# Optimization experiments

Hardware: AMD Instinct MI355X
Metric: run time of the kernel (lower is better)

## Reference

```python
import jax, jax.numpy as jnp
import numpy as np

NQ = 4
NL = 3
# Z-expectation sign table: state axis order = wire order, reshape(-1) => wire 0 is MSB
_bits = (np.arange(2 ** NQ)[:, None] >> np.arange(NQ - 1, -1, -1)) & 1
Z_SIGNS = jnp.asarray((1 - 2 * _bits).astype(np.float32))  # (16, 4)
_CNOT = jnp.asarray(np.array([[1, 0, 0, 0], [0, 1, 0, 0], [0, 0, 0, 1], [0, 0, 1, 0]],
                             dtype=np.complex64).reshape(2, 2, 2, 2))


def _rx(t):
    c = jnp.cos(t / 2).astype(jnp.complex64)
    s = (-1j) * jnp.sin(t / 2).astype(jnp.complex64)
    return jnp.stack([jnp.stack([c, s]), jnp.stack([s, c])])


def _rot(phi, theta, omega):
    # PennyLane Rot = RZ(omega) @ RY(theta) @ RZ(phi)
    ez = jnp.exp(-0.5j * phi.astype(jnp.complex64))
    zero = jnp.zeros_like(ez)
    rz1 = jnp.stack([jnp.stack([ez, zero]), jnp.stack([zero, jnp.conj(ez)])])
    c = jnp.cos(theta / 2).astype(jnp.complex64)
    s = jnp.sin(theta / 2).astype(jnp.complex64)
    ry = jnp.stack([jnp.stack([c, -s]), jnp.stack([s, c])])
    eo = jnp.exp(-0.5j * omega.astype(jnp.complex64))
    rz2 = jnp.stack([jnp.stack([eo, zero]), jnp.stack([zero, jnp.conj(eo)])])
    return rz2 @ ry @ rz1


def _apply1(state, U, wire):
    state = jnp.tensordot(U, state, axes=[[1], [wire]])
    return jnp.moveaxis(state, 0, wire)


def _apply_cnot(state, c, t):
    state = jnp.tensordot(_CNOT, state, axes=[[2, 3], [c, t]])
    return jnp.moveaxis(state, [0, 1], [c, t])


def _circuit(x4, qw):
    state = jnp.zeros((2,) * NQ, jnp.complex64).at[(0,) * NQ].set(1.0)
    for i in range(NQ):
        state = _apply1(state, _rx(x4[i]), i)
    for layer in range(NL):
        for q in range(NQ):
            state = _apply1(state, _rot(qw[layer, q, 0], qw[layer, q, 1], qw[layer, q, 2]), q)
        for q in range(NQ - 1):
            state = _apply_cnot(state, q, q + 1)
    probs = jnp.abs(state.reshape(-1)) ** 2  # (16,)
    return probs @ Z_SIGNS  # (NQ,) PauliZ expectations


def setup_inputs() -> dict:
    key = jax.random.key(0)
    ks = jax.random.split(key, 16)
    D, H1, H2, L = 2048, 128, 64, 32
    B = 16384
    s = 0.02
    return {
        "x": jax.random.normal(ks[0], (B, D), jnp.float32),
        "enc_w0": jax.random.normal(ks[1], (D, H1), jnp.float32) * s,
        "enc_b0": jnp.zeros((H1,), jnp.float32),
        "enc_w1": jax.random.normal(ks[2], (H1, H2), jnp.float32) * s,
        "enc_b1": jnp.zeros((H2,), jnp.float32),
        "enc_w2": jax.random.normal(ks[3], (H2, L), jnp.float32) * s,
        "enc_b2": jnp.zeros((L,), jnp.float32),
        "qw": jax.random.normal(ks[4], (NL, NQ, 3), jnp.float32),
        "dec_w0": jax.random.normal(ks[5], (NQ, H2), jnp.float32) * s,
        "dec_b0": jnp.zeros((H2,), jnp.float32),
        "dec_w1": jax.random.normal(ks[6], (H2, H1), jnp.float32) * s,
        "dec_b1": jnp.zeros((H1,), jnp.float32),
        "dec_w2": jax.random.normal(ks[7], (H1, D), jnp.float32) * s,
        "dec_b2": jnp.zeros((D,), jnp.float32),
    }


def reference(x, enc_w0, enc_b0, enc_w1, enc_b1, enc_w2, enc_b2, qw,
              dec_w0, dec_b0, dec_w1, dec_b1, dec_w2, dec_b2):
    # Encoder (eval mode: dropout is identity)
    h = jax.nn.relu(x @ enc_w0 + enc_b0)
    h = jax.nn.relu(h @ enc_w1 + enc_b1)
    latent = h @ enc_w2 + enc_b2  # (B, 32)
    # Quantum refinement: circuit only reads latent[:, :NQ]
    refined = jax.vmap(lambda xi: _circuit(xi, qw))(latent[:, :NQ]).astype(jnp.float32)  # (B, 4)
    # Decoder
    h = jax.nn.relu(refined @ dec_w0 + dec_b0)
    h = jax.nn.relu(h @ dec_w1 + dec_b1)
    return h @ dec_w2 + dec_b2
```

## Files before the change

### kernel.cpp

```cpp
#include <hip/hip_runtime.h>
#include <hip/hip_bf16.h>

typedef __attribute__((ext_vector_type(8))) short short8;
typedef __attribute__((ext_vector_type(4))) float f32x4;

#define DEVI __device__ __forceinline__

DEVI unsigned short f2bf(float f) {
    union { float f; unsigned u; } v; v.f = f;
    unsigned r = v.u + 0x7FFFu + ((v.u >> 16) & 1u);
    return (unsigned short)(r >> 16);
}

DEVI unsigned cvtpk_bf16(float lo, float hi) {
    float2 t; t.x = lo; t.y = hi;
    __hip_bfloat162 h = __float22bfloat162_rn(t);
    union { __hip_bfloat162 h; unsigned u; } c; c.h = h;
    return c.u;
}

DEVI void gload_lds16(const void* g, void* l) {
    __builtin_amdgcn_global_load_lds(
        (const __attribute__((address_space(1))) unsigned int*)(unsigned long long)g,
        (__attribute__((address_space(3))) unsigned int*)(unsigned int)(unsigned long long)l,
        16, 0, 0);
}

DEVI void run_circuit(const float lat[4], const float* __restrict__ qw, float out4[4])
{
    float cw[4], sw[4];
#pragma unroll
    for (int w = 0; w < 4; ++w) sincosf(0.5f * lat[w], &sw[w], &cw[w]);

    float sr[16], si[16];
#pragma unroll
    for (int s = 0; s < 16; ++s) {
        float mag = 1.f; int p = 0;
#pragma unroll
        for (int w = 0; w < 4; ++w) {
            int b = (s >> (3 - w)) & 1;
            mag *= b ? sw[w] : cw[w];
            p += b;
        }
        p &= 3;
        sr[s] = (p == 0) ? mag : ((p == 2) ? -mag : 0.f);
        si[s] = (p == 1) ? -mag : ((p == 3) ? mag : 0.f);
    }

#pragma unroll
    for (int L = 0; L < 3; ++L) {
#pragma unroll
        for (int q = 0; q < 4; ++q) {
            const float* gq = qw + (L * 4 + q) * 3;
            float phi = gq[0], th = gq[1], om = gq[2];
            float ct, st;
            sincosf(0.5f * th, &st, &ct);
            float ap = 0.5f * (phi + om), am = 0.5f * (phi - om);
            float cap, sap, cam, sam;
            sincosf(ap, &sap, &cap);
            sincosf(am, &sam, &cam);
            float u00r =  ct * cap, u00i = -ct * sap;
            float u01r = -st * cam, u01i = -st * sam;
            float u10r =  st * cam, u10i = -st * sam;
            float u11r =  ct * cap, u11i =  ct * sap;
            int bm = 8 >> q;
#pragma unroll
            for (int i = 0; i < 16; ++i) {
                if (i & bm) continue;
                int j = i | bm;
                float ar = sr[i], ai = si[i], br = sr[j], bi = si[j];
                sr[i] = u00r*ar - u00i*ai + u01r*br - u01i*bi;
                si[i] = u00r*ai + u00i*ar + u01r*bi + u01i*br;
                sr[j] = u10r*ar - u10i*ai + u11r*br - u11i*bi;
                si[j] = u10r*ai + u10i*ar + u11r*bi + u11i*br;
            }
        }
#pragma unroll
        for (int q = 0; q < 3; ++q) {
            int cm = 8 >> q, tm = 8 >> (q + 1);
#pragma unroll
            for (int i = 0; i < 16; ++i) {
                if ((i & cm) && !(i & tm)) {
                    int j = i | tm;
                    float tr = sr[i]; sr[i] = sr[j]; sr[j] = tr;
                    float ti = si[i]; si[i] = si[j]; si[j] = ti;
                }
            }
        }
    }
#pragma unroll
    for (int q = 0; q < 4; ++q) {
        int bm = 8 >> q;
        float e = 0.f;
#pragma unroll
        for (int i = 0; i < 16; ++i) {
            float p = sr[i]*sr[i] + si[i]*si[i];
            e += (i & bm) ? -p : p;
        }
        out4[q] = e;
    }
}

__global__ void prep_kernel(const float* __restrict__ ew0, const float* __restrict__ ew1,
                            const float* __restrict__ dw1, const float* __restrict__ dw2,
                            unsigned short* __restrict__ wsb)
{
    int i = blockIdx.x * 256 + threadIdx.x;
    if (i < 262144) {
        int n = i >> 11, k = i & 2047;
        wsb[i] = f2bf(ew0[k * 128 + n]);
    } else if (i < 270336) {
        int t = i - 262144; int n = t >> 7, k = t & 127;
        wsb[i] = f2bf(ew1[k * 64 + n]);
    } else if (i < 278528) {
        int t = i - 270336; int n = t >> 6, k = t & 63;
        wsb[i] = f2bf(dw1[k * 128 + n]);
    } else if (i < 540672) {
        int t = i - 278528; int n = t >> 7, k = t & 127;
        wsb[i] = f2bf(dw2[k * 2048 + n]);
    }
}

__launch_bounds__(256, 2)
__global__ void enc_a_kernel(const float* __restrict__ x,
                             const unsigned short* __restrict__ w0T,
                             const float* __restrict__ b0g,
                             unsigned short* __restrict__ h1)
{
    __shared__ __align__(16) char smem[49152];

    const int tid = threadIdx.x;
    const int lane = tid & 63;
    const int wv = tid >> 6;
    const int wm = wv >> 1, wn = wv & 1;
    const int l16 = lane & 15, lq = lane >> 4;
    const int m0 = blockIdx.x * 32;

    const int rA0 = wv * 8 + (lane >> 4);
    const int rA1 = wv * 8 + 4 + (lane >> 4);
    const int slA0 = (lane & 15) ^ ((rA0 & 7) << 1);
    const int slA1 = (lane & 15) ^ ((rA1 & 7) << 1);
    const char* sA0 = (const char*)(x + (long)(m0 + rA0) * 2048 + slA0 * 4);
    const char* sA1 = (const char*)(x + (long)(m0 + rA1) * 2048 + slA1 * 4);
    const int rB0 = wv * 32 +  0 + (lane >> 3);
    const int rB1 = wv * 32 +  8 + (lane >> 3);
    const int rB2 = wv * 32 + 16 + (lane >> 3);
    const int rB3 = wv * 32 + 24 + (lane >> 3);
    const char* sB0 = (const char*)(w0T + rB0 * 2048 + ((lane & 7) ^ (rB0 & 7)) * 8);
    const char* sB1 = (const char*)(w0T + rB1 * 2048 + ((lane & 7) ^ (rB1 & 7)) * 8);
    const char* sB2 = (const char*)(w0T + rB2 * 2048 + ((lane & 7) ^ (rB2 & 7)) * 8);
    const char* sB3 = (const char*)(w0T + rB3 * 2048 + ((lane & 7) ^ (rB3 & 7)) * 8);
    const int aoff0 = wv * 2048;
    const int aoff1 = wv * 2048 + 1024;
    const int boff0 = wv * 4096;
    const int boff1 = wv * 4096 + 1024;
    const int boff2 = wv * 4096 + 2048;
    const int boff3 = wv * 4096 + 3072;

    auto issue = [&](int cur) {
        char* Ab = smem + (cur ? 8192 : 0);
        char* Bb = smem + (cur ? 32768 : 16384);
        gload_lds16(sA0, Ab + aoff0); sA0 += 256;
        gload_lds16(sA1, Ab + aoff1); sA1 += 256;
        gload_lds16(sB0, Bb + boff0); sB0 += 128;
        gload_lds16(sB1, Bb + boff1); sB1 += 128;
        gload_lds16(sB2, Bb + boff2); sB2 += 128;
        gload_lds16(sB3, Bb + boff3); sB3 += 128;
    };

    f32x4 acc[4];
#pragma unroll
    for (int b = 0; b < 4; ++b) acc[b] = (f32x4)(0.f);

    const int arow = wm * 16 + l16;
    const unsigned aswz = (unsigned)((arow & 7) << 1);

    issue(0);
    __syncthreads();

    for (int t = 0; t < 32; ++t) {
        if (t < 31) issue((t + 1) & 1);
        const char* Ab = smem + ((t & 1) ? 8192 : 0);
        const char* Bb = smem + ((t & 1) ? 32768 : 16384);
#pragma unroll
        for (int kk = 0; kk < 2; ++kk) {
            const int c = kk * 8 + lq * 2;
            const char* ap = Ab + arow * 256 + (((unsigned)c ^ aswz) << 4);
            float4 f0 = *(const float4*)ap;
            float4 f1 = *(const float4*)(ap + 16);
            union { unsigned u[4]; short8 s; } pk;
            pk.u[0] = cvtpk_bf16(f0.x, f0.y);
            pk.u[1] = cvtpk_bf16(f0.z, f0.w);
            pk.u[2] = cvtpk_bf16(f1.x, f1.y);
            pk.u[3] = cvtpk_bf16(f1.z, f1.w);
            short8 aF = pk.s;
#pragma unroll
            for (int fn = 0; fn < 4; ++fn) {
                int n = wn * 64 + fn * 16 + l16;
                short8 bF = *(const short8*)(Bb + n * 128 + (((kk * 4 + lq) ^ (n & 7)) << 4));
                acc[fn] = __builtin_amdgcn_mfma_f32_16x16x32_bf16(aF, bF, acc[fn], 0, 0, 0);
            }
        }
        __syncthreads();
    }

    float b0v[4];
#pragma unroll
    for (int fn = 0; fn < 4; ++fn) b0v[fn] = b0g[wn * 64 + fn * 16 + l16];
#pragma unroll
    for (int fn = 0; fn < 4; ++fn)
#pragma unroll
        for (int r = 0; r < 4; ++r) {
            int row = m0 + wm * 16 + lq * 4 + r;
            int col = wn * 64 + fn * 16 + l16;
            h1[row * 128 + col] = f2bf(fmaxf(acc[fn][r] + b0v[fn], 0.f));
        }
}

__launch_bounds__(256, 2)
__global__ void enc_b_kernel(const unsigned short* __restrict__ h1,
                             const unsigned short* __restrict__ w1eT,
                             const float* __restrict__ b1e,
                             const float* __restrict__ w2e,
                             const float* __restrict__ b2e,
                             const float* __restrict__ qw,
                             const float* __restrict__ w0d,
                             const float* __restrict__ b0d,
                             const unsigned short* __restrict__ w1dT,
                             const float* __restrict__ b1d,
                             unsigned short* __restrict__ g)
{
    __shared__ __align__(16) char smem[76288];
    char* const HA   = smem;
    char* const W1E  = smem + 16384;
    char* const W1D  = smem + 32768;
    float* const H2  = (float*)(smem + 49152);
    char* const HD   = smem + 65792;
    float* const W2C = (float*)(smem + 73984);
    float* const W0D = (float*)(smem + 75008);
    float* const B0D = (float*)(smem + 76032);

    const int tid = threadIdx.x;
    const int lane = tid & 63;
    const int wv = tid >> 6;
    const int wm = wv >> 1, wn = wv & 1;
    const int l16 = lane & 15, lq = lane >> 4;
    const int m0 = blockIdx.x * 64;

    {
        const int r16 = wv * 16 + (lane >> 4);
        const int s16 = lane & 15;
        const int r8  = wv * 32 + (lane >> 3);
        const int s8  = lane & 7;
#pragma unroll
        for (int i = 0; i < 4; ++i) {
            int row = r16 + i * 4;
            gload_lds16(h1 + (m0 + row) * 128 + ((s16 ^ (row & 7)) * 8),
                        HA + wv * 4096 + i * 1024);
        }
#pragma unroll
        for (int i = 0; i < 4; ++i) {
            int row = r16 + i * 4;
            gload_lds16(w1eT + row * 128 + ((s16 ^ (row & 7)) * 8),
                        W1E + wv * 4096 + i * 1024);
        }
#pragma unroll
        for (int i = 0; i < 4; ++i) {
            int row = r8 + i * 8;
            gload_lds16(w1dT + row * 64 + ((s8 ^ (row & 7)) * 8),
                        W1D + wv * 4096 + i * 1024);
        }
    }
    W2C[tid] = w2e[(tid >> 2) * 32 + (tid & 3)];
    W0D[tid] = w0d[tid];
    if (tid < 64) B0D[tid] = b0d[tid];
    __syncthreads();

    f32x4 acc2[2][2];
#pragma unroll
    for (int a = 0; a < 2; ++a)
#pragma unroll
        for (int b = 0; b < 2; ++b) acc2[a][b] = (f32x4)(0.f);
#pragma unroll
    for (int kk = 0; kk < 4; ++kk) {
        short8 aF[2], bF[2];
#pragma unroll
        for (int fm = 0; fm < 2; ++fm) {
            int row = wm * 32 + fm * 16 + l16;
            aF[fm] = *(const short8*)(HA + row * 256 + (((kk * 4 + lq) ^ (row & 7)) << 4));
        }
#pragma unroll
        for (int fn = 0; fn < 2; ++fn) {
            int n = wn * 32 + fn * 16 + l16;
            bF[fn] = *(const short8*)(W1E + n * 256 + (((kk * 4 + lq) ^ (n & 7)) << 4));
        }
#pragma unroll
        for (int fm = 0; fm < 2; ++fm)
#pragma unroll
            for (int fn = 0; fn < 2; ++fn)
                acc2[fm][fn] = __builtin_amdgcn_mfma_f32_16x16x32_bf16(aF[fm], bF[fn], acc2[fm][fn], 0, 0, 0);
    }
    {
        float b1v[2];
#pragma unroll
        for (int fn = 0; fn < 2; ++fn) b1v[fn] = b1e[wn * 32 + fn * 16 + l16];
#pragma unroll
        for (int fm = 0; fm < 2; ++fm)
#pragma unroll
            for (int fn = 0; fn < 2; ++fn)
#pragma unroll
                for (int r = 0; r < 4; ++r) {
                    int row = wm * 32 + fm * 16 + lq * 4 + r;
                    int col = wn * 32 + fn * 16 + l16;
                    H2[row * 65 + col] = fmaxf(acc2[fm][fn][r] + b1v[fn], 0.f);
                }
    }
    __syncthreads();

    if (tid < 64) {
        float lat[4];
#pragma unroll
        for (int j = 0; j < 4; ++j) lat[j] = b2e[j];
        const float* h2row = H2 + tid * 65;
#pragma unroll 8
        for (int k = 0; k < 64; ++k) {
            float hv = h2row[k];
#pragma unroll
            for (int j = 0; j < 4; ++j) lat[j] = fmaf(hv, W2C[k * 4 + j], lat[j]);
        }
        float o4[4];
        run_circuit(lat, qw, o4);
#pragma unroll
        for (int s = 0; s < 8; ++s) {
            uint4 pk;
            unsigned tmp[4];
#pragma unroll
            for (int p = 0; p < 4; ++p) {
                int c0 = s * 8 + p * 2;
                float v0 = fmaxf(o4[0]*W0D[c0]     + o4[1]*W0D[64+c0]   + o4[2]*W0D[128+c0]   + o4[3]*W0D[192+c0]   + B0D[c0],   0.f);
                float v1 = fmaxf(o4[0]*W0D[c0+1]   + o4[1]*W0D[64+c0+1] + o4[2]*W0D[128+c0+1] + o4[3]*W0D[192+c0+1] + B0D[c0+1], 0.f);
                tmp[p] = (unsigned)f2bf(v0) | ((unsigned)f2bf(v1) << 16);
            }
            pk.x = tmp[0]; pk.y = tmp[1]; pk.z = tmp[2]; pk.w = tmp[3];
            *(uint4*)(HD + tid * 128 + ((s ^ (tid & 7)) << 4)) = pk;
        }
    }
    __syncthreads();

    f32x4 accg[2][4];
#pragma unroll
    for (int a = 0; a < 2; ++a)
#pragma unroll
        for (int b = 0; b < 4; ++b) accg[a][b] = (f32x4)(0.f);
#pragma unroll
    for (int kk = 0; kk < 2; ++kk) {
        short8 aF[2], bF[4];
#pragma unroll
        for (int fm = 0; fm < 2; ++fm) {
            int row = wm * 32 + fm * 16 + l16;
            aF[fm] = *(const short8*)(HD + row * 128 + (((kk * 4 + lq) ^ (row & 7)) << 4));
        }
#pragma unroll
        for (int fn = 0; fn < 4; ++fn) {
            int n = wn * 64 + fn * 16 + l16;
            bF[fn] = *(const short8*)(W1D + n * 128 + (((kk * 4 + lq) ^ (n & 7)) << 4));
        }
#pragma unroll
        for (int fm = 0; fm < 2; ++fm)
#pragma unroll
            for (int fn = 0; fn < 4; ++fn)
                accg[fm][fn] = __builtin_amdgcn_mfma_f32_16x16x32_bf16(aF[fm], bF[fn], accg[fm][fn], 0, 0, 0);
    }
    {
        float b1v[4];
#pragma unroll
        for (int fn = 0; fn < 4; ++fn) b1v[fn] = b1d[wn * 64 + fn * 16 + l16];
#pragma unroll
        for (int fm = 0; fm < 2; ++fm)
#pragma unroll
            for (int fn = 0; fn < 4; ++fn)
#pragma unroll
                for (int r = 0; r < 4; ++r) {
                    int row = wm * 32 + fm * 16 + lq * 4 + r;
                    int col = wn * 64 + fn * 16 + l16;
                    g[(m0 + row) * 128 + col] = f2bf(fmaxf(accg[fm][fn][r] + b1v[fn], 0.f));
                }
    }
}

__launch_bounds__(256, 2)
__global__ void dec_b_kernel(const unsigned short* __restrict__ g,
                             const unsigned short* __restrict__ w2T,
                             const float* __restrict__ b2g,
                             float* __restrict__ out)
{
    __shared__ __align__(16) char smem[49152];
    char* const GA = smem;
    char* const WB = smem + 16384;

    const int tid = threadIdx.x;
    const int lane = tid & 63;
    const int wv = tid >> 6;
    const int wm = wv >> 1, wn = wv & 1;
    const int l16 = lane & 15, lq = lane >> 4;
    const int bid = blockIdx.x;
    const int n0 = (bid & 15) * 128;
    const int m0 = (bid >> 4) * 64;

    {
        const int rl = (lane >> 4);
        const int s16 = lane & 15;
#pragma unroll
        for (int i = 0; i < 4; ++i) {
            int row = wv * 16 + i * 4 + rl;
            gload_lds16(g + (m0 + row) * 128 + ((s16 ^ (row & 7)) * 8),
                        GA + wv * 4096 + i * 1024);
        }
#pragma unroll
        for (int i = 0; i < 8; ++i) {
            int row = wv * 32 + i * 4 + rl;
            gload_lds16(w2T + (n0 + row) * 128 + ((s16 ^ (row & 7)) * 8),
                        WB + wv * 8192 + i * 1024);
        }
    }
    __syncthreads();

    f32x4 a3[2][4];
#pragma unroll
    for (int a = 0; a < 2; ++a)
#pragma unroll
        for (int b = 0; b < 4; ++b) a3[a][b] = (f32x4)(0.f);
#pragma unroll
    for (int kk = 0; kk < 4; ++kk) {
        short8 aF[2], bF[4];
#pragma unroll
        for (int fm = 0; fm < 2; ++fm) {
            int row = wm * 32 + fm * 16 + l16;
            aF[fm] = *(const short8*)(GA + row * 256 + (((kk * 4 + lq) ^ (row & 7)) << 4));
        }
#pragma unroll
        for (int fn = 0; fn < 4; ++fn) {
            int n = wn * 64 + fn * 16 + l16;
            bF[fn] = *(const short8*)(WB + n * 256 + (((kk * 4 + lq) ^ (n & 7)) << 4));
        }
#pragma unroll
        for (int fm = 0; fm < 2; ++fm)
#pragma unroll
            for (int fn = 0; fn < 4; ++fn)
                a3[fm][fn] = __builtin_amdgcn_mfma_f32_16x16x32_bf16(aF[fm], bF[fn], a3[fm][fn], 0, 0, 0);
    }
    float b2v[4];
#pragma unroll
    for (int fn = 0; fn < 4; ++fn) b2v[fn] = b2g[n0 + wn * 64 + fn * 16 + l16];
#pragma unroll
    for (int fm = 0; fm < 2; ++fm)
#pragma unroll
        for (int fn = 0; fn < 4; ++fn)
#pragma unroll
            for (int r = 0; r < 4; ++r) {
                int row = m0 + wm * 32 + fm * 16 + lq * 4 + r;
                int col = n0 + wn * 64 + fn * 16 + l16;
                out[(long)row * 2048 + col] = a3[fm][fn][r] + b2v[fn];
            }
}

__launch_bounds__(256, 1)
__global__ void enc_kernel(const float* __restrict__ x,
                           const unsigned short* __restrict__ w0T,
                           const unsigned short* __restrict__ w1T,
                           const float* __restrict__ b0g,
                           const float* __restrict__ b1g,
                           const float* __restrict__ w2g,
                           const float* __restrict__ b2g,
                           const float* __restrict__ qw,
                           float* __restrict__ refined)
{
    __shared__ __align__(16) char smem[50432];
    char* const Abuf0 = smem;
    char* const Abuf1 = smem + 8192;
    char* const Bbuf0 = smem + 16384;
    char* const Bbuf1 = smem + 32768;
    char* const H1 = smem;
    char* const W1 = smem + 16384;
    float* const H2 = (float*)(smem + 32768);
    float* const W2C = (float*)(smem + 49408);

    const int tid = threadIdx.x;
    const int lane = tid & 63;
    const int wv = tid >> 6;
    const int wm = wv >> 1, wn = wv & 1;
    const int l16 = lane & 15, lq = lane >> 4;
    const int m0 = blockIdx.x * 64;

    const int ar = tid >> 4;
    const int ac4 = tid & 15;
    const int bn = tid >> 3;
    const int bs = tid & 7;

    const float* xg = x + m0 * 2048;
    W2C[tid] = w2g[(tid >> 2) * 32 + (tid & 3)];

    f32x4 acc[2][4];
#pragma unroll
    for (int a = 0; a < 2; ++a)
#pragma unroll
        for (int b = 0; b < 4; ++b) acc[a][b] = (f32x4)(0.f);

    float4 aL[4];
    uint4 bL[4];

    auto issue_loads = [&](int k0) {
#pragma unroll
        for (int j = 0; j < 4; ++j)
            aL[j] = *(const float4*)(xg + (ar + 16 * j) * 2048 + k0 + ac4 * 4);
#pragma unroll
        for (int j = 0; j < 4; ++j)
            bL[j] = *(const uint4*)(w0T + (bn + 32 * j) * 2048 + k0 + bs * 8);
    };
    auto write_lds = [&](int buf) {
        char* A = buf ? Abuf1 : Abuf0;
        char* B = buf ? Bbuf1 : Bbuf0;
#pragma unroll
        for (int j = 0; j < 4; ++j) {
            int r = ar + 16 * j;
            unsigned p0 = (unsigned)f2bf(aL[j].x) | ((unsigned)f2bf(aL[j].y) << 16);
            unsigned p1 = (unsigned)f2bf(aL[j].z) | ((unsigned)f2bf(aL[j].w) << 16);
            unsigned long long pk = (unsigned long long)p0 | ((unsigned long long)p1 << 32);
            *(unsigned long long*)(A + r * 128 + ((((ac4 >> 1) ^ (r & 7)) << 4) | ((ac4 & 1) << 3))) = pk;
        }
#pragma unroll
        for (int j = 0; j < 4; ++j) {
            int n = bn + 32 * j;
            *(uint4*)(B + n * 128 + ((bs ^ (n & 7)) << 4)) = bL[j];
        }
    };
    auto compute_tile = [&](int buf) {
        char* A = buf ? Abuf1 : Abuf0;
        char* B = buf ? Bbuf1 : Bbuf0;
#pragma unroll
        for (int kk = 0; kk < 2; ++kk) {
            short8 aF[2], bF[4];
#pragma unroll
            for (int fm = 0; fm < 2; ++fm) {
                int row = wm * 32 + fm * 16 + l16;
                aF[fm] = *(const short8*)(A + row * 128 + (((kk * 4 + lq) ^ (row & 7)) << 4));
            }
#pragma unroll
            for (int fn = 0; fn < 4; ++fn) {
                int n = wn * 64 + fn * 16 + l16;
                bF[fn] = *(const short8*)(B + n * 128 + (((kk * 4 + lq) ^ (n & 7)) << 4));
            }
#pragma unroll
            for (int fm = 0; fm < 2; ++fm)
#pragma unroll
                for (int fn = 0; fn < 4; ++fn)
                    acc[fm][fn] = __builtin_amdgcn_mfma_f32_16x16x32_bf16(aF[fm], bF[fn], acc[fm][fn], 0, 0, 0);
        }
    };

    issue_loads(0);
    write_lds(0);
    __syncthreads();
#pragma unroll 2
    for (int it = 0; it < 32; ++it) {
        if (it < 31) issue_loads((it + 1) * 64);
        compute_tile(it & 1);
        if (it < 31) {
            write_lds((it + 1) & 1);
            __syncthreads();
        }
    }
    __syncthreads();

    uint4 wL[4];
#pragma unroll
    for (int j = 0; j < 4; ++j) {
        int u = tid + 256 * j, n = u >> 4, s = u & 15;
        wL[j] = *(const uint4*)(w1T + n * 128 + s * 8);
    }
    float b0v[4];
#pragma unroll
    for (int fn = 0; fn < 4; ++fn) b0v[fn] = b0g[wn * 64 + fn * 16 + l16];
#pragma unroll
    for (int fm = 0; fm < 2; ++fm)
#pragma unroll
        for (int fn = 0; fn < 4; ++fn)
#pragma unroll
            for (int r = 0; r < 4; ++r) {
                int row = wm * 32 + fm * 16 + lq * 4 + r;
                int col = wn * 64 + fn * 16 + l16;
                float v = fmaxf(acc[fm][fn][r] + b0v[fn], 0.f);
                *(unsigned short*)(H1 + row * 256 + ((((col >> 3) ^ (row & 7)) << 4) | ((col & 7) << 1))) = f2bf(v);
            }
#pragma unroll
    for (int j = 0; j < 4; ++j) {
        int u = tid + 256 * j, n = u >> 4, s = u & 15;
        *(uint4*)(W1 + n * 256 + ((s ^ (n & 7)) << 4)) = wL[j];
    }
    __syncthreads();

    f32x4 acc2[2][2];
#pragma unroll
    for (int a = 0; a < 2; ++a)
#pragma unroll
        for (int b = 0; b < 2; ++b) acc2[a][b] = (f32x4)(0.f);
#pragma unroll
    for (int kk = 0; kk < 4; ++kk) {
        short8 aF[2], bF[2];
#pragma unroll
        for (int fm = 0; fm < 2; ++fm) {
            int row = wm * 32 + fm * 16 + l16;
            aF[fm] = *(const short8*)(H1 + row * 256 + (((kk * 4 + lq) ^ (row & 7)) << 4));
        }
#pragma unroll
        for (int fn = 0; fn < 2; ++fn) {
            int n = wn * 32 + fn * 16 + l16;
            bF[fn] = *(const short8*)(W1 + n * 256 + (((kk * 4 + lq) ^ (n & 7)) << 4));
        }
#pragma unroll
        for (int fm = 0; fm < 2; ++fm)
#pragma unroll
            for (int fn = 0; fn < 2; ++fn)
                acc2[fm][fn] = __builtin_amdgcn_mfma_f32_16x16x32_bf16(aF[fm], bF[fn], acc2[fm][fn], 0, 0, 0);
    }
    float b1v[2];
#pragma unroll
    for (int fn = 0; fn < 2; ++fn) b1v[fn] = b1g[wn * 32 + fn * 16 + l16];
#pragma unroll
    for (int fm = 0; fm < 2; ++fm)
#pragma unroll
        for (int fn = 0; fn < 2; ++fn)
#pragma unroll
            for (int r = 0; r < 4; ++r) {
                int row = wm * 32 + fm * 16 + lq * 4 + r;
                int col = wn * 32 + fn * 16 + l16;
                H2[row * 65 + col] = fmaxf(acc2[fm][fn][r] + b1v[fn], 0.f);
            }
    __syncthreads();

    if (tid < 64) {
        float lat[4];
#pragma unroll
        for (int j = 0; j < 4; ++j) lat[j] = b2g[j];
        const float* h2row = H2 + tid * 65;
#pragma unroll 8
        for (int k = 0; k < 64; ++k) {
            float hv = h2row[k];
#pragma unroll
            for (int j = 0; j < 4; ++j) lat[j] = fmaf(hv, W2C[k * 4 + j], lat[j]);
        }
        float o4[4];
        run_circuit(lat, qw, o4);
        *(float4*)(refined + (m0 + tid) * 4) = make_float4(o4[0], o4[1], o4[2], o4[3]);
    }
}

__launch_bounds__(256, 1)
__global__ void dec_kernel(const float* __restrict__ refined,
                           const float* __restrict__ w0g,
                           const float* __restrict__ b0g,
                           const unsigned short* __restrict__ w1T,
                           const float* __restrict__ b1g,
                           const unsigned short* __restrict__ w2T,
                           const float* __restrict__ b2g,
                           float* __restrict__ out)
{
    __shared__ __align__(16) char smem[106496];
    char* const HA  = smem;
    char* const W1  = smem + 8192;
    char* const GA  = smem + 24576;
    char* const W2a = smem + 40960;
    char* const W2b = smem + 73728;

    const int tid = threadIdx.x;
    const int lane = tid & 63;
    const int wv = tid >> 6;
    const int wm = wv >> 1, wn = wv & 1;
    const int l16 = lane & 15, lq = lane >> 4;
    const int m0 = blockIdx.x * 64;

    uint4 w1L[4];
#pragma unroll
    for (int j = 0; j < 4; ++j)
        w1L[j] = *(const uint4*)(w1T + ((tid >> 3) + 32 * j) * 64 + (tid & 7) * 8);

    const int hr = tid >> 2, hc0 = (tid & 3) * 16;
    float4 rf = *(const float4*)(refined + (m0 + hr) * 4);
    unsigned short hb[16];
#pragma unroll
    for (int i = 0; i < 16; ++i) {
        int c = hc0 + i;
        float v = rf.x * w0g[c] + rf.y * w0g[64 + c] + rf.z * w0g[128 + c] + rf.w * w0g[192 + c] + b0g[c];
        hb[i] = f2bf(fmaxf(v, 0.f));
    }
#pragma unroll
    for (int half = 0; half < 2; ++half) {
        uint4 pk;
        pk.x = (unsigned)hb[half*8+0] | ((unsigned)hb[half*8+1] << 16);
        pk.y = (unsigned)hb[half*8+2] | ((unsigned)hb[half*8+3] << 16);
        pk.z = (unsigned)hb[half*8+4] | ((unsigned)hb[half*8+5] << 16);
        pk.w = (unsigned)hb[half*8+6] | ((unsigned)hb[half*8+7] << 16);
        int slot = (tid & 3) * 2 + half;
        *(uint4*)(HA + hr * 128 + ((slot ^ (hr & 7)) << 4)) = pk;
    }
#pragma unroll
    for (int j = 0; j < 4; ++j) {
        int n = (tid >> 3) + 32 * j;
        *(uint4*)(W1 + n * 128 + (((tid & 7) ^ (n & 7)) << 4)) = w1L[j];
    }
    uint4 w2L[8];
    const int w2n = tid >> 4, w2s = tid & 15;
#pragma unroll
    for (int j = 0; j < 8; ++j)
        w2L[j] = *(const uint4*)(w2T + (w2n + 16 * j) * 128 + w2s * 8);
    __syncthreads();

    f32x4 accg[2][4];
#pragma unroll
    for (int a = 0; a < 2; ++a)
#pragma unroll
        for (int b = 0; b < 4; ++b) accg[a][b] = (f32x4)(0.f);
#pragma unroll
    for (int kk = 0; kk < 2; ++kk) {
        short8 aF[2], bF[4];
#pragma unroll
        for (int fm = 0; fm < 2; ++fm) {
            int row = wm * 32 + fm * 16 + l16;
            aF[fm] = *(const short8*)(HA + row * 128 + (((kk * 4 + lq) ^ (row & 7)) << 4));
        }
#pragma unroll
        for (int fn = 0; fn < 4; ++fn) {
            int n = wn * 64 + fn * 16 + l16;
            bF[fn] = *(const short8*)(W1 + n * 128 + (((kk * 4 + lq) ^ (n & 7)) << 4));
        }
#pragma unroll
        for (int fm = 0; fm < 2; ++fm)
#pragma unroll
            for (int fn = 0; fn < 4; ++fn)
                accg[fm][fn] = __builtin_amdgcn_mfma_f32_16x16x32_bf16(aF[fm], bF[fn], accg[fm][fn], 0, 0, 0);
    }
    float b1v[4];
#pragma unroll
    for (int fn = 0; fn < 4; ++fn) b1v[fn] = b1g[wn * 64 + fn * 16 + l16];
#pragma unroll
    for (int fm = 0; fm < 2; ++fm)
#pragma unroll
        for (int fn = 0; fn < 4; ++fn)
#pragma unroll
            for (int r = 0; r < 4; ++r) {
                int row = wm * 32 + fm * 16 + lq * 4 + r;
                int col = wn * 64 + fn * 16 + l16;
                float v = fmaxf(accg[fm][fn][r] + b1v[fn], 0.f);
                *(unsigned short*)(GA + row * 256 + ((((col >> 3) ^ (row & 7)) << 4) | ((col & 7) << 1))) = f2bf(v);
            }
#pragma unroll
    for (int j = 0; j < 8; ++j) {
        int n = w2n + 16 * j;
        *(uint4*)(W2a + n * 256 + ((w2s ^ (n & 7)) << 4)) = w2L[j];
    }
    __syncthreads();

#pragma unroll 2
    for (int nc = 0; nc < 16; ++nc) {
        char* Wc = (nc & 1) ? W2b : W2a;
        if (nc < 15) {
#pragma unroll
            for (int j = 0; j < 8; ++j)
                w2L[j] = *(const uint4*)(w2T + ((nc + 1) * 128 + w2n + 16 * j) * 128 + w2s * 8);
        }
        f32x4 a3[2][4];
#pragma unroll
        for (int a = 0; a < 2; ++a)
#pragma unroll
            for (int b = 0; b < 4; ++b) a3[a][b] = (f32x4)(0.f);
#pragma unroll
        for (int kk = 0; kk < 4; ++kk) {
            short8 aF[2], bF[4];
#pragma unroll
            for (int fm = 0; fm < 2; ++fm) {
                int row = wm * 32 + fm * 16 + l16;
                aF[fm] = *(const short8*)(GA + row * 256 + (((kk * 4 + lq) ^ (row & 7)) << 4));
            }
#pragma unroll
            for (int fn = 0; fn < 4; ++fn) {
                int n = wn * 64 + fn * 16 + l16;
                bF[fn] = *(const short8*)(Wc + n * 256 + (((kk * 4 + lq) ^ (n & 7)) << 4));
            }
#pragma unroll
            for (int fm = 0; fm < 2; ++fm)
#pragma unroll
                for (int fn = 0; fn < 4; ++fn)
                    a3[fm][fn] = __builtin_amdgcn_mfma_f32_16x16x32_bf16(aF[fm], bF[fn], a3[fm][fn], 0, 0, 0);
        }
        int n0 = nc * 128;
        float b2v[4];
#pragma unroll
        for (int fn = 0; fn < 4; ++fn) b2v[fn] = b2g[n0 + wn * 64 + fn * 16 + l16];
#pragma unroll
        for (int fm = 0; fm < 2; ++fm)
#pragma unroll
            for (int fn = 0; fn < 4; ++fn)
#pragma unroll
                for (int r = 0; r < 4; ++r) {
                    int row = m0 + wm * 32 + fm * 16 + lq * 4 + r;
                    int col = n0 + wn * 64 + fn * 16 + l16;
                    out[row * 2048 + col] = a3[fm][fn][r] + b2v[fn];
                }
        if (nc < 15) {
            char* Wn = (nc & 1) ? W2a : W2b;
#pragma unroll
            for (int j = 0; j < 8; ++j) {
                int n = w2n + 16 * j;
                *(uint4*)(Wn + n * 256 + ((w2s ^ (n & 7)) << 4)) = w2L[j];
            }
            __syncthreads();
        }
    }
}

extern "C" void kernel_launch(void* const* d_in, const int* in_sizes, int n_in,
                              void* d_out, int out_size, void* d_ws, size_t ws_size,
                              hipStream_t stream)
{
    (void)in_sizes; (void)n_in; (void)out_size;
    const float* x      = (const float*)d_in[0];
    const float* enc_w0 = (const float*)d_in[1];
    const float* enc_b0 = (const float*)d_in[2];
    const float* enc_w1 = (const float*)d_in[3];
    const float* enc_b1 = (const float*)d_in[4];
    const float* enc_w2 = (const float*)d_in[5];
    const float* enc_b2 = (const float*)d_in[6];
    const float* qw     = (const float*)d_in[7];
    const float* dec_w0 = (const float*)d_in[8];
    const float* dec_b0 = (const float*)d_in[9];
    const float* dec_w1 = (const float*)d_in[10];
    const float* dec_b1 = (const float*)d_in[11];
    const float* dec_w2 = (const float*)d_in[12];
    const float* dec_b2 = (const float*)d_in[13];

    unsigned short* wsb = (unsigned short*)d_ws;

    prep_kernel<<<2112, 256, 0, stream>>>(enc_w0, enc_w1, dec_w1, dec_w2, wsb);

    if (ws_size >= 9469952) {
        unsigned short* h1 = wsb + 540672;
        unsigned short* gbuf = wsb + 2637824;
        enc_a_kernel<<<512, 256, 0, stream>>>(x, wsb, enc_b0, h1);
        enc_b_kernel<<<256, 256, 0, stream>>>(h1, wsb + 262144, enc_b1, enc_w2, enc_b2, qw,
                                              dec_w0, dec_b0, wsb + 270336, dec_b1, gbuf);
        dec_b_kernel<<<4096, 256, 0, stream>>>(gbuf, wsb + 278528, dec_b2, (float*)d_out);
    } else {
        float* refined = (float*)((char*)d_ws + 1081344);
        enc_kernel<<<256, 256, 0, stream>>>(x, wsb, wsb + 262144,
                                            enc_b0, enc_b1, enc_w2, enc_b2, qw, refined);
        dec_kernel<<<256, 256, 0, stream>>>(refined, dec_w0, dec_b0, wsb + 270336,
                                            dec_b1, wsb + 278528, dec_b2, (float*)d_out);
    }
}
```

Before: 98.81 us.

## Triple-buffer encoder first-layer GEMM loads with explicit vmcnt waits

The first encoder GEMM moves from a double-buffered LDS pipeline to a three-stage ring, keeping two tiles of global-to-LDS loads in flight while computing on the third. The implicit full waits in __syncthreads are replaced by explicit s_waitcnt vmcnt counts plus raw barriers, so outstanding prefetches are not drained every iteration. LDS use rises from 48KB to 72KB per block, which may limit the two-blocks-per-CU occupancy target and relies on the hand-counted vmcnt values being correct.

Result: no change. 100.6 us (+1.9%).

```diff
diff --git a/kernel.cpp b/kernel.cpp
--- a/kernel.cpp
+++ b/kernel.cpp
@@ -127,7 +127,7 @@
                              const float* __restrict__ b0g,
                              unsigned short* __restrict__ h1)
 {
-    __shared__ __align__(16) char smem[49152];
+    __shared__ __align__(16) char smem[73728];
 
     const int tid = threadIdx.x;
     const int lane = tid & 63;
@@ -157,9 +157,9 @@
     const int boff2 = wv * 4096 + 2048;
     const int boff3 = wv * 4096 + 3072;
 
-    auto issue = [&](int cur) {
-        char* Ab = smem + (cur ? 8192 : 0);
-        char* Bb = smem + (cur ? 32768 : 16384);
+    auto issue = [&](int buf) {
+        char* Ab = smem + buf * 8192;
+        char* Bb = smem + 24576 + buf * 16384;
         gload_lds16(sA0, Ab + aoff0); sA0 += 256;
         gload_lds16(sA1, Ab + aoff1); sA1 += 256;
         gload_lds16(sB0, Bb + boff0); sB0 += 128;
@@ -175,13 +175,9 @@
     const int arow = wm * 16 + l16;
     const unsigned aswz = (unsigned)((arow & 7) << 1);
 
-    issue(0);
-    __syncthreads();
-
-    for (int t = 0; t < 32; ++t) {
-        if (t < 31) issue((t + 1) & 1);
-        const char* Ab = smem + ((t & 1) ? 8192 : 0);
-        const char* Bb = smem + ((t & 1) ? 32768 : 16384);
+    auto compute = [&](int buf) {
+        const char* Ab = smem + buf * 8192;
+        const char* Bb = smem + 24576 + buf * 16384;
 #pragma unroll
         for (int kk = 0; kk < 2; ++kk) {
             const int c = kk * 8 + lq * 2;
@@ -201,7 +197,26 @@
                 acc[fn] = __builtin_amdgcn_mfma_f32_16x16x32_bf16(aF, bF, acc[fn], 0, 0, 0);
             }
         }
-        __syncthreads();
+    };
+
+    issue(0);
+    issue(1);
+
+    int buf = 0;
+    for (int t = 0; t < 32; ++t) {
+        if (t < 30) {
+            int nb = buf + 2; if (nb >= 3) nb -= 3;
+            issue(nb);
+            asm volatile("s_waitcnt vmcnt(12)" ::: "memory");
+        } else if (t == 30) {
+            asm volatile("s_waitcnt vmcnt(6)" ::: "memory");
+        } else {
+            asm volatile("s_waitcnt vmcnt(0)" ::: "memory");
+        }
+        __builtin_amdgcn_s_barrier();
+        compute(buf);
+        __builtin_amdgcn_s_barrier();
+        ++buf; if (buf >= 3) buf -= 3;
     }
 
     float b0v[4];
```
